# Kernel optimization log

Hardware: AMD Instinct MI355X
Metric: run time of the kernel (lower is better)

## Reference

```python
import jax, jax.numpy as jnp
import numpy as np

B, C, D, H, W = 4, 256, 16, 16, 16
REDUCTION = 8
CR = C // REDUCTION  # q/k channel dim = 32


def setup_inputs() -> dict:
    key = jax.random.key(0)
    k1, k2, k3, k4, k5, k6 = jax.random.split(key, 6)
    x = jax.random.normal(k1, (B, C, D, H, W), dtype=jnp.float32)
    # 1x1x1 conv weights are just [out_ch, in_ch] matrices
    Wq = jax.random.normal(k2, (CR, C), dtype=jnp.float32) * (1.0 / np.sqrt(C))
    Wk = jax.random.normal(k3, (CR, C), dtype=jnp.float32) * (1.0 / np.sqrt(C))
    Wv = jax.random.normal(k4, (C, C), dtype=jnp.float32) * (1.0 / np.sqrt(C))
    Wo = jax.random.normal(k5, (C, C), dtype=jnp.float32) * (1.0 / np.sqrt(C))
    gamma = jnp.zeros((1,), dtype=jnp.float32) + 0.5  # nonzero so output depends on attention
    return {"x": x, "Wq": Wq, "Wk": Wk, "Wv": Wv, "Wo": Wo, "gamma": gamma}


def reference(x, Wq, Wk, Wv, Wo, gamma):
    b, c, d, h, w = x.shape
    n = d * h * w
    scale = Wq.shape[0] ** -0.5  # (channels // reduction) ** -0.5
    xf = x.reshape(b, c, n)                      # [B, C, N]
    q = jnp.einsum('oc,bcn->bon', Wq, xf)        # [B, CR, N]
    k = jnp.einsum('oc,bcn->bon', Wk, xf)        # [B, CR, N]
    v = jnp.einsum('oc,bcn->bon', Wv, xf)        # [B, C, N]
    attn = jax.nn.softmax(jnp.einsum('bcn,bcm->bnm', q, k) * scale, axis=-1)  # [B, N, N]
    out = jnp.einsum('bcm,bnm->bcn', v, attn)    # v @ attn^T -> [B, C, N]
    out = jnp.einsum('oc,bcn->bon', Wo, out)     # output 1x1x1 conv
    out = out.reshape(b, c, d, h, w)
    return gamma[0] * out + x
```

## Files before the change

### kernel.cpp

```cpp
#include <hip/hip_runtime.h>
#include <hip/hip_bf16.h>

#define BATCH 4
#define CH 256
#define CRD 32
#define NN 4096

typedef __bf16 bf16x8 __attribute__((ext_vector_type(8)));
typedef float floatx4 __attribute__((ext_vector_type(4)));
typedef float floatx16 __attribute__((ext_vector_type(16)));
typedef unsigned short ushort4v __attribute__((ext_vector_type(4)));
typedef unsigned short ushort8v __attribute__((ext_vector_type(8)));
typedef unsigned int uint2v __attribute__((ext_vector_type(2)));
typedef unsigned int uint4v __attribute__((ext_vector_type(4)));

static __device__ __forceinline__ unsigned short f2bf(float f) {
    __bf16 h = (__bf16)f;
    return __builtin_bit_cast(unsigned short, h);
}
static __device__ __forceinline__ float bf2f(unsigned short h) {
    return __uint_as_float((unsigned int)h << 16);
}


__global__ __launch_bounds__(256) void wconv_kernel(
    const float* __restrict__ Wq, const float* __restrict__ Wk,
    const float* __restrict__ Wv, const float* __restrict__ Wo,
    unsigned short* __restrict__ What, unsigned short* __restrict__ WobF)
{
    const int o = blockIdx.x;
    const int t = threadIdx.x;
    float scale = 1.0f;
    const float* src;
    if (o < 32)      { src = Wq + o * 256;
                       scale = 0.17677669529663687f * 1.4426950408889634f; }
    else if (o < 64) { src = Wk + (o - 32) * 256; }
    else             { src = Wv + (o - 64) * 256; }
    const int mb = o >> 5;
    const size_t idx = ((size_t)(mb * 16 + (t >> 4)) * 64
                        + (o & 31) + 32 * ((t >> 3) & 1)) * 8 + (t & 7);
    What[idx] = f2bf(src[t] * scale);
    if (o < 256) {
        const size_t i2 = ((size_t)((o >> 5) * 16 + (t >> 4)) * 64
                           + (o & 31) + 32 * ((t >> 3) & 1)) * 8 + (t & 7);
        WobF[i2] = f2bf(Wo[o * 256 + t]);
    }
}

static __device__ __forceinline__ uint4v hmerge(
    const ushort4v& xp, const ushort4v& yp, int h)
{
    uint2v xd = __builtin_bit_cast(uint2v, xp);
    uint2v yd = __builtin_bit_cast(uint2v, yp);
    unsigned int px0 = (unsigned int)__shfl_xor((int)xd[0], 32);
    unsigned int px1 = (unsigned int)__shfl_xor((int)xd[1], 32);
    unsigned int py0 = (unsigned int)__shfl_xor((int)yd[0], 32);
    unsigned int py1 = (unsigned int)__shfl_xor((int)yd[1], 32);
    uint4v st;
    st[0] = h ? py0 : xd[0];
    st[1] = h ? py1 : xd[1];
    st[2] = h ? yd[0] : px0;
    st[3] = h ? yd[1] : px1;
    return st;
}

__global__ __launch_bounds__(256, 2) void qkv_kernel(
    const float* __restrict__ x, const unsigned short* __restrict__ What,
    unsigned short* __restrict__ qh, unsigned short* __restrict__ kh,
    unsigned short* __restrict__ vh)
{
    __shared__ __align__(16) unsigned short xf[16 * 512];

    const int t = threadIdx.x;
    const int w = t >> 6;
    const int l = t & 63;
    const int l31 = l & 31;
    const int h = l >> 5;
    const int nt = blockIdx.x, b = blockIdx.y;
    const int n0 = nt * 32;

    {
        const float* xb = x + (size_t)(b * CH) * NN + n0;
        const int n = t & 31;
        const int cq = t >> 5;
        #pragma unroll
        for (int p = 0; p < 8; ++p) {
            int c = p * 32 + cq * 4;
            float v0 = xb[(size_t)(c + 0) * NN + n];
            float v1 = xb[(size_t)(c + 1) * NN + n];
            float v2 = xb[(size_t)(c + 2) * NN + n];
            float v3 = xb[(size_t)(c + 3) * NN + n];
            ushort4v u4;
            u4[0] = f2bf(v0); u4[1] = f2bf(v1); u4[2] = f2bf(v2); u4[3] = f2bf(v3);
            int addr = ((2 * p + (cq >> 2)) * 64 + n + 32 * ((cq >> 1) & 1)) * 8
                       + 4 * (cq & 1);
            *(ushort4v*)&xf[addr] = u4;
        }
    }
    __syncthreads();

    const int mb0 = w, mb1 = w + 4, mb2 = w + 8;
    floatx16 acc0, acc1, acc2;
    #pragma unroll
    for (int i = 0; i < 16; ++i) { acc0[i] = 0.f; acc1[i] = 0.f; acc2[i] = 0.f; }

    for (int kblk = 0; kblk < 16; ++kblk) {
        bf16x8 bf = *(const bf16x8*)&xf[kblk * 512 + l * 8];
        bf16x8 a0 = *(const bf16x8*)(What + ((size_t)(mb0 * 16 + kblk) * 64 + l) * 8);
        bf16x8 a1 = *(const bf16x8*)(What + ((size_t)(mb1 * 16 + kblk) * 64 + l) * 8);
        acc0 = __builtin_amdgcn_mfma_f32_32x32x16_bf16(a0, bf, acc0, 0, 0, 0);
        acc1 = __builtin_amdgcn_mfma_f32_32x32x16_bf16(a1, bf, acc1, 0, 0, 0);
        if (w < 2) {
            bf16x8 a2 = *(const bf16x8*)(What + ((size_t)(mb2 * 16 + kblk) * 64 + l) * 8);
            acc2 = __builtin_amdgcn_mfma_f32_32x32x16_bf16(a2, bf, acc2, 0, 0, 0);
        }
    }

    auto store_qk = [&](unsigned short* dst, const floatx16& a) {
        size_t base = (size_t)(b * 128 + nt) * 1024;
        #pragma unroll
        for (int sb = 0; sb < 2; ++sb) {
            ushort4v xp, yp;
            #pragma unroll
            for (int i = 0; i < 4; ++i) {
                xp[i] = f2bf(a[8 * sb + i]);
                yp[i] = f2bf(a[8 * sb + 4 + i]);
            }
            uint4v st = hmerge(xp, yp, h);
            *(uint4v*)(dst + base + (size_t)sb * 512 + (size_t)l * 8) = st;
        }
    };

    if (w == 0)      store_qk(qh, acc0);
    else if (w == 1) store_qk(kh, acc0);

    __syncthreads();

    auto store_v_lds = [&](int cblk, const floatx16& a) {
        const int chunk = cblk * 2 + (l31 >> 4);
        const int hib = (l31 >> 3) & 1;
        #pragma unroll
        for (int r = 0; r < 16; ++r) {
            int rowo = (r & 3) + 8 * (r >> 2) + 4 * h;
            int unit = chunk * 64 + hib * 32 + rowo;
            int pu = unit ^ ((unit >> 5) & 7);
            xf[pu * 8 + (l31 & 7)] = f2bf(a[r]);
        }
    };

    if (w >= 2) store_v_lds(w - 2, acc0);
    store_v_lds(w + 2, acc1);
    if (w < 2) store_v_lds(w + 6, acc2);

    __syncthreads();

    #pragma unroll
    for (int p = 0; p < 4; ++p) {
        int Lu = p * 256 + t;
        int pu = Lu ^ ((Lu >> 5) & 7);
        uint4v d = *(const uint4v*)&xf[pu * 8];
        int chunk = Lu >> 6;
        int cblk = chunk >> 1, sub = chunk & 1;
        size_t dst = (((size_t)b * 8 + cblk) * 256 + nt * 2 + sub) * 512
                     + (size_t)(Lu & 63) * 8;
        *(uint4v*)(vh + dst) = d;
    }
}

#define SM_M0 12.0f

__global__ __launch_bounds__(512, 4) void attn_kernel(
    const unsigned short* __restrict__ qh, const unsigned short* __restrict__ kh,
    const unsigned short* __restrict__ vh, unsigned short* __restrict__ Opart,
    float* __restrict__ ml)
{
    __shared__ unsigned short p_lds[2 * 16 * 64 * 8];
    __shared__ float psum_s[8][32];

    const int t = threadIdx.x;
    const int w = t >> 6;
    const int l = t & 63;
    const int l31 = l & 31;
    const int h = l >> 5;
    const int wk = w & 3;
    const int hq = w >> 2;

    const int lin = blockIdx.x + ((int)blockIdx.y << 6) + ((int)blockIdx.z << 7);
    const int combo = lin & 7;
    const int gp = lin >> 3;
    const int ks = combo & 1;
    const int b  = combo >> 1;
    const int g0 = 2 * gp, g1 = 2 * gp + 1;

    const unsigned short* qB = qh + (size_t)(b * 128 + (hq ? g1 : g0)) * 1024;
    const unsigned short* kB = kh + (size_t)b * 128 * 1024;
    const unsigned short* vB = vh + (size_t)b * 8 * 256 * 512;

    bf16x8 qf0 = *(const bf16x8*)(qB + l * 8);
    bf16x8 qf1 = *(const bf16x8*)(qB + 512 + l * 8);

    bf16x8 kf0 = *(const bf16x8*)(kB + (size_t)(ks * 64 + wk) * 1024 + l * 8);
    bf16x8 kf1 = *(const bf16x8*)(kB + (size_t)(ks * 64 + wk) * 1024 + 512 + l * 8);

    float l_loc = 0.f;
    floatx16 acc_a, acc_b;
    #pragma unroll
    for (int i = 0; i < 16; ++i) { acc_a[i] = 0.f; acc_b[i] = 0.f; }

    for (int it = 0; it < 16; ++it) {
        const int pbase = (it & 1) << 13;

        floatx16 sacc;
        #pragma unroll
        for (int i = 0; i < 16; ++i) sacc[i] = 0.f;
        __builtin_amdgcn_s_setprio(1);
        sacc = __builtin_amdgcn_mfma_f32_32x32x16_bf16(kf0, qf0, sacc, 0, 0, 0);
        sacc = __builtin_amdgcn_mfma_f32_32x32x16_bf16(kf1, qf1, sacc, 0, 0, 0);
        __builtin_amdgcn_s_setprio(0);

        float pv[16];
        #pragma unroll
        for (int r = 0; r < 16; ++r) pv[r] = __builtin_exp2f(sacc[r] - SM_M0);
        float s0 = (pv[0] + pv[1]) + (pv[2] + pv[3]);
        float s1 = (pv[4] + pv[5]) + (pv[6] + pv[7]);
        float s2 = (pv[8] + pv[9]) + (pv[10] + pv[11]);
        float s3 = (pv[12] + pv[13]) + (pv[14] + pv[15]);
        l_loc += (s0 + s1) + (s2 + s3);
        #pragma unroll
        for (int rg = 0; rg < 4; ++rg) {
            ushort4v pk;
            #pragma unroll
            for (int i = 0; i < 4; ++i) pk[i] = f2bf(pv[rg * 4 + i]);
            int idx = pbase
                    + ((hq * 8 + 2 * wk + (rg >> 1)) * 64
                       + l31 + 32 * (rg & 1)) * 8 + 4 * h;
            *(ushort4v*)&p_lds[idx] = pk;
        }
        if (it < 15) {
            const unsigned short* kn = kB + (size_t)(ks * 64 + (it + 1) * 4 + wk) * 1024;
            kf0 = *(const bf16x8*)(kn + l * 8);
            kf1 = *(const bf16x8*)(kn + 512 + l * 8);
        }
        const unsigned short* v0b = vB + ((size_t)w * 256 + (ks * 16 + it) * 8) * 512;
        bf16x8 va0 = *(const bf16x8*)(v0b + 0 * 512 + l * 8);
        bf16x8 va1 = *(const bf16x8*)(v0b + 1 * 512 + l * 8);
        bf16x8 va2 = *(const bf16x8*)(v0b + 2 * 512 + l * 8);
        bf16x8 va3 = *(const bf16x8*)(v0b + 3 * 512 + l * 8);
        bf16x8 va4 = *(const bf16x8*)(v0b + 4 * 512 + l * 8);
        bf16x8 va5 = *(const bf16x8*)(v0b + 5 * 512 + l * 8);
        bf16x8 va6 = *(const bf16x8*)(v0b + 6 * 512 + l * 8);
        bf16x8 va7 = *(const bf16x8*)(v0b + 7 * 512 + l * 8);

        __syncthreads();

        bf16x8 pa = *(const bf16x8*)&p_lds[pbase + l * 8];
        bf16x8 pb = *(const bf16x8*)&p_lds[pbase + 4096 + l * 8];
        #pragma unroll
        for (int s = 0; s < 8; ++s) {
            bf16x8 vcur = (s == 0) ? va0 : (s == 1) ? va1 : (s == 2) ? va2
                        : (s == 3) ? va3 : (s == 4) ? va4 : (s == 5) ? va5
                        : (s == 6) ? va6 : va7;
            bf16x8 pa_n, pb_n;
            if (s < 7) {
                pa_n = *(const bf16x8*)&p_lds[pbase + ((s + 1) * 64 + l) * 8];
                pb_n = *(const bf16x8*)&p_lds[pbase + 4096 + ((s + 1) * 64 + l) * 8];
            }
            __builtin_amdgcn_s_setprio(1);
            acc_a = __builtin_amdgcn_mfma_f32_32x32x16_bf16(vcur, pa, acc_a, 0, 0, 0);
            acc_b = __builtin_amdgcn_mfma_f32_32x32x16_bf16(vcur, pb, acc_b, 0, 0, 0);
            __builtin_amdgcn_s_setprio(0);
            pa = pa_n; pb = pb_n;
        }
    }

    float lt = l_loc + __shfl_xor(l_loc, 32);
    if (h == 0) psum_s[w][l31] = lt;
    __syncthreads();

    if (w == 0 && h == 0) {
        float l_run = (psum_s[0][l31] + psum_s[1][l31])
                    + (psum_s[2][l31] + psum_s[3][l31]);
        ml[((size_t)(b * 128 + g0) * 2 + ks) * 32 + l31] = l_run;
    }
    if (w == 4 && h == 0) {
        float l_run = (psum_s[4][l31] + psum_s[5][l31])
                    + (psum_s[6][l31] + psum_s[7][l31]);
        ml[((size_t)(b * 128 + g1) * 2 + ks) * 32 + l31] = l_run;
    }

    unsigned short* opa = Opart + ((size_t)((b * 128 + g0) * 2 + ks)) * 8192;
    unsigned short* opb = Opart + ((size_t)((b * 128 + g1) * 2 + ks)) * 8192;
    #pragma unroll
    for (int ct = 0; ct < 2; ++ct) {
        const floatx16& a = ct ? acc_b : acc_a;
        unsigned short* op = ct ? opb : opa;
        #pragma unroll
        for (int sb = 0; sb < 2; ++sb) {
            ushort4v xp, yp;
            #pragma unroll
            for (int i = 0; i < 4; ++i) {
                xp[i] = f2bf(a[8 * sb + i]);
                yp[i] = f2bf(a[8 * sb + 4 + i]);
            }
            uint4v st = hmerge(xp, yp, h);
            int sP = 2 * w + sb;
            *(uint4v*)(op + ((size_t)sP * 64 + l) * 8) = st;
        }
    }
}

__global__ __launch_bounds__(256, 2) void out_kernel(
    const unsigned short* __restrict__ Opart, const float* __restrict__ ml,
    const unsigned short* __restrict__ WobF, const float* __restrict__ x,
    const float* __restrict__ gamma, float* __restrict__ out)
{
    const int t = threadIdx.x;
    const int w = t >> 6;
    const int l = t & 63;
    const int l31 = l & 31;
    const int h = l >> 5;
    const int qt = blockIdx.x, b = blockIdx.y;

    const size_t slot2 = (size_t)(b * 128 + qt) * 2;
    float l0 = ml[(slot2 + 0) * 32 + l31];
    float l1 = ml[(slot2 + 1) * 32 + l31];
    float rL = 1.0f / (l0 + l1);

    const unsigned short* o0 = Opart + (slot2 + 0) * 8192;
    const unsigned short* o1 = Opart + (slot2 + 1) * 8192;

    floatx16 a0[2], a1[2];
    #pragma unroll
    for (int m = 0; m < 2; ++m)
        #pragma unroll
        for (int i = 0; i < 16; ++i) { a0[m][i] = 0.f; a1[m][i] = 0.f; }

    #pragma unroll 2
    for (int s = 0; s < 16; ++s) {
        bf16x8 f0 = *(const bf16x8*)(o0 + (s * 64 + l) * 8);
        bf16x8 f1 = *(const bf16x8*)(o1 + (s * 64 + l) * 8);
        #pragma unroll
        for (int m = 0; m < 2; ++m) {
            int mt = 2 * w + m;
            bf16x8 af = *(const bf16x8*)(WobF + ((size_t)(mt * 16 + s) * 64 + l) * 8);
            a0[m] = __builtin_amdgcn_mfma_f32_32x32x16_bf16(af, f0, a0[m], 0, 0, 0);
            a1[m] = __builtin_amdgcn_mfma_f32_32x32x16_bf16(af, f1, a1[m], 0, 0, 0);
        }
    }

    const float gm = gamma[0];
    #pragma unroll
    for (int m = 0; m < 2; ++m)
        #pragma unroll
        for (int r = 0; r < 16; ++r) {
            float v = (a0[m][r] + a1[m][r]) * rL;
            int o = (2 * w + m) * 32 + (r & 3) + 8 * (r >> 2) + 4 * h;
            int n = qt * 32 + l31;
            size_t oi = ((size_t)(b * 256 + o)) * NN + n;
            out[oi] = gm * v + x[oi];
        }
}

extern "C" void kernel_launch(void* const* d_in, const int* in_sizes, int n_in,
                              void* d_out, int out_size, void* d_ws, size_t ws_size,
                              hipStream_t stream)
{
    const float* x     = (const float*)d_in[0];
    const float* Wq    = (const float*)d_in[1];
    const float* Wk    = (const float*)d_in[2];
    const float* Wv    = (const float*)d_in[3];
    const float* Wo    = (const float*)d_in[4];
    const float* gamma = (const float*)d_in[5];
    float* out = (float*)d_out;

    char* wsb = (char*)d_ws;
    unsigned short* qh    = (unsigned short*)(wsb);
    unsigned short* kh    = (unsigned short*)(wsb + (1u << 20));
    unsigned short* vh    = (unsigned short*)(wsb + (2u << 20));
    unsigned short* What  = (unsigned short*)(wsb + (10u << 20));
    unsigned short* WobF  = (unsigned short*)(wsb + (10u << 20) + (256u << 10));
    unsigned short* Opart = (unsigned short*)(wsb + (11u << 20));
    float*          ml    = (float*)         (wsb + (45u << 20));

    wconv_kernel<<<320, 256, 0, stream>>>(Wq, Wk, Wv, Wo, What, WobF);

    dim3 g1(128, BATCH);
    qkv_kernel<<<g1, 256, 0, stream>>>(x, What, qh, kh, vh);

    dim3 g2(64, 2, BATCH);
    attn_kernel<<<g2, 512, 0, stream>>>(qh, kh, vh, Opart, ml);

    dim3 g3(128, BATCH);
    out_kernel<<<g3, 256, 0, stream>>>(Opart, ml, WobF, x, gamma, out);
}
```

Baseline: 150.9 us.

## Spread QKV and output projection work across more waves and blocks

The QKV kernel now launches 640 threads (10 waves), so each wave computes a single 32-row tile instead of two or three. The x load and V writeback are split across 512 threads. The output kernel's grid is doubled along a new y dimension so each wave handles one output tile instead of two. The intent is more parallelism and occupancy for these small kernels, in exchange for redundant Opart and x loads across blocks and larger block sizes.

```diff
diff --git a/kernel.cpp b/kernel.cpp
--- a/kernel.cpp
+++ b/kernel.cpp
@@ -64,7 +64,7 @@
     return st;
 }
 
-__global__ __launch_bounds__(256, 2) void qkv_kernel(
+__global__ __launch_bounds__(640, 4) void qkv_kernel(
     const float* __restrict__ x, const unsigned short* __restrict__ What,
     unsigned short* __restrict__ qh, unsigned short* __restrict__ kh,
     unsigned short* __restrict__ vh)
@@ -79,41 +79,34 @@
     const int nt = blockIdx.x, b = blockIdx.y;
     const int n0 = nt * 32;
 
-    {
+    if (t < 512) {
         const float* xb = x + (size_t)(b * CH) * NN + n0;
         const int n = t & 31;
         const int cq = t >> 5;
         #pragma unroll
-        for (int p = 0; p < 8; ++p) {
-            int c = p * 32 + cq * 4;
+        for (int p = 0; p < 4; ++p) {
+            int c = p * 64 + cq * 4;
             float v0 = xb[(size_t)(c + 0) * NN + n];
             float v1 = xb[(size_t)(c + 1) * NN + n];
             float v2 = xb[(size_t)(c + 2) * NN + n];
             float v3 = xb[(size_t)(c + 3) * NN + n];
             ushort4v u4;
             u4[0] = f2bf(v0); u4[1] = f2bf(v1); u4[2] = f2bf(v2); u4[3] = f2bf(v3);
-            int addr = ((2 * p + (cq >> 2)) * 64 + n + 32 * ((cq >> 1) & 1)) * 8
+            int addr = ((4 * p + (cq >> 2)) * 64 + n + 32 * ((cq >> 1) & 1)) * 8
                        + 4 * (cq & 1);
             *(ushort4v*)&xf[addr] = u4;
         }
     }
     __syncthreads();
 
-    const int mb0 = w, mb1 = w + 4, mb2 = w + 8;
-    floatx16 acc0, acc1, acc2;
-    #pragma unroll
-    for (int i = 0; i < 16; ++i) { acc0[i] = 0.f; acc1[i] = 0.f; acc2[i] = 0.f; }
+    floatx16 acc;
+    #pragma unroll
+    for (int i = 0; i < 16; ++i) acc[i] = 0.f;
 
     for (int kblk = 0; kblk < 16; ++kblk) {
         bf16x8 bf = *(const bf16x8*)&xf[kblk * 512 + l * 8];
-        bf16x8 a0 = *(const bf16x8*)(What + ((size_t)(mb0 * 16 + kblk) * 64 + l) * 8);
-        bf16x8 a1 = *(const bf16x8*)(What + ((size_t)(mb1 * 16 + kblk) * 64 + l) * 8);
-        acc0 = __builtin_amdgcn_mfma_f32_32x32x16_bf16(a0, bf, acc0, 0, 0, 0);
-        acc1 = __builtin_amdgcn_mfma_f32_32x32x16_bf16(a1, bf, acc1, 0, 0, 0);
-        if (w < 2) {
-            bf16x8 a2 = *(const bf16x8*)(What + ((size_t)(mb2 * 16 + kblk) * 64 + l) * 8);
-            acc2 = __builtin_amdgcn_mfma_f32_32x32x16_bf16(a2, bf, acc2, 0, 0, 0);
-        }
+        bf16x8 af = *(const bf16x8*)(What + ((size_t)(w * 16 + kblk) * 64 + l) * 8);
+        acc = __builtin_amdgcn_mfma_f32_32x32x16_bf16(af, bf, acc, 0, 0, 0);
     }
 
     auto store_qk = [&](unsigned short* dst, const floatx16& a) {
@@ -131,12 +124,13 @@
         }
     };
 
-    if (w == 0)      store_qk(qh, acc0);
-    else if (w == 1) store_qk(kh, acc0);
+    if (w == 0)      store_qk(qh, acc);
+    else if (w == 1) store_qk(kh, acc);
 
     __syncthreads();
 
-    auto store_v_lds = [&](int cblk, const floatx16& a) {
+    if (w >= 2) {
+        const int cblk = w - 2;
         const int chunk = cblk * 2 + (l31 >> 4);
         const int hib = (l31 >> 3) & 1;
         #pragma unroll
@@ -144,26 +138,24 @@
             int rowo = (r & 3) + 8 * (r >> 2) + 4 * h;
             int unit = chunk * 64 + hib * 32 + rowo;
             int pu = unit ^ ((unit >> 5) & 7);
-            xf[pu * 8 + (l31 & 7)] = f2bf(a[r]);
-        }
-    };
-
-    if (w >= 2) store_v_lds(w - 2, acc0);
-    store_v_lds(w + 2, acc1);
-    if (w < 2) store_v_lds(w + 6, acc2);
+            xf[pu * 8 + (l31 & 7)] = f2bf(acc[r]);
+        }
+    }
 
     __syncthreads();
 
-    #pragma unroll
-    for (int p = 0; p < 4; ++p) {
-        int Lu = p * 256 + t;
-        int pu = Lu ^ ((Lu >> 5) & 7);
-        uint4v d = *(const uint4v*)&xf[pu * 8];
-        int chunk = Lu >> 6;
-        int cblk = chunk >> 1, sub = chunk & 1;
-        size_t dst = (((size_t)b * 8 + cblk) * 256 + nt * 2 + sub) * 512
-                     + (size_t)(Lu & 63) * 8;
-        *(uint4v*)(vh + dst) = d;
+    if (t < 512) {
+        #pragma unroll
+        for (int p = 0; p < 2; ++p) {
+            int Lu = p * 512 + t;
+            int pu = Lu ^ ((Lu >> 5) & 7);
+            uint4v d = *(const uint4v*)&xf[pu * 8];
+            int chunk = Lu >> 6;
+            int cblk = chunk >> 1, sub = chunk & 1;
+            size_t dst = (((size_t)b * 8 + cblk) * 256 + nt * 2 + sub) * 512
+                         + (size_t)(Lu & 63) * 8;
+            *(uint4v*)(vh + dst) = d;
+        }
     }
 }
 
@@ -309,7 +301,7 @@
     }
 }
 
-__global__ __launch_bounds__(256, 2) void out_kernel(
+__global__ __launch_bounds__(256, 4) void out_kernel(
     const unsigned short* __restrict__ Opart, const float* __restrict__ ml,
     const unsigned short* __restrict__ WobF, const float* __restrict__ x,
     const float* __restrict__ gamma, float* __restrict__ out)
@@ -319,7 +311,8 @@
     const int l = t & 63;
     const int l31 = l & 31;
     const int h = l >> 5;
-    const int qt = blockIdx.x, b = blockIdx.y;
+    const int qt = blockIdx.x, mhalf = blockIdx.y, b = blockIdx.z;
+    const int mt = mhalf * 4 + w;
 
     const size_t slot2 = (size_t)(b * 128 + qt) * 2;
     float l0 = ml[(slot2 + 0) * 32 + l31];
@@ -329,36 +322,27 @@
     const unsigned short* o0 = Opart + (slot2 + 0) * 8192;
     const unsigned short* o1 = Opart + (slot2 + 1) * 8192;
 
-    floatx16 a0[2], a1[2];
-    #pragma unroll
-    for (int m = 0; m < 2; ++m)
-        #pragma unroll
-        for (int i = 0; i < 16; ++i) { a0[m][i] = 0.f; a1[m][i] = 0.f; }
-
-    #pragma unroll 2
+    floatx16 a0, a1;
+    #pragma unroll
+    for (int i = 0; i < 16; ++i) { a0[i] = 0.f; a1[i] = 0.f; }
+
     for (int s = 0; s < 16; ++s) {
         bf16x8 f0 = *(const bf16x8*)(o0 + (s * 64 + l) * 8);
         bf16x8 f1 = *(const bf16x8*)(o1 + (s * 64 + l) * 8);
-        #pragma unroll
-        for (int m = 0; m < 2; ++m) {
-            int mt = 2 * w + m;
-            bf16x8 af = *(const bf16x8*)(WobF + ((size_t)(mt * 16 + s) * 64 + l) * 8);
-            a0[m] = __builtin_amdgcn_mfma_f32_32x32x16_bf16(af, f0, a0[m], 0, 0, 0);
-            a1[m] = __builtin_amdgcn_mfma_f32_32x32x16_bf16(af, f1, a1[m], 0, 0, 0);
-        }
+        bf16x8 af = *(const bf16x8*)(WobF + ((size_t)(mt * 16 + s) * 64 + l) * 8);
+        a0 = __builtin_amdgcn_mfma_f32_32x32x16_bf16(af, f0, a0, 0, 0, 0);
+        a1 = __builtin_amdgcn_mfma_f32_32x32x16_bf16(af, f1, a1, 0, 0, 0);
     }
 
     const float gm = gamma[0];
     #pragma unroll
-    for (int m = 0; m < 2; ++m)
-        #pragma unroll
-        for (int r = 0; r < 16; ++r) {
-            float v = (a0[m][r] + a1[m][r]) * rL;
-            int o = (2 * w + m) * 32 + (r & 3) + 8 * (r >> 2) + 4 * h;
-            int n = qt * 32 + l31;
-            size_t oi = ((size_t)(b * 256 + o)) * NN + n;
-            out[oi] = gm * v + x[oi];
-        }
+    for (int r = 0; r < 16; ++r) {
+        float v = (a0[r] + a1[r]) * rL;
+        int o = mt * 32 + (r & 3) + 8 * (r >> 2) + 4 * h;
+        int n = qt * 32 + l31;
+        size_t oi = ((size_t)(b * 256 + o)) * NN + n;
+        out[oi] = gm * v + x[oi];
+    }
 }
 
 extern "C" void kernel_launch(void* const* d_in, const int* in_sizes, int n_in,
@@ -385,11 +369,11 @@
     wconv_kernel<<<320, 256, 0, stream>>>(Wq, Wk, Wv, Wo, What, WobF);
 
     dim3 g1(128, BATCH);
-    qkv_kernel<<<g1, 256, 0, stream>>>(x, What, qh, kh, vh);
+    qkv_kernel<<<g1, 640, 0, stream>>>(x, What, qh, kh, vh);
 
     dim3 g2(64, 2, BATCH);
     attn_kernel<<<g2, 512, 0, stream>>>(qh, kh, vh, Opart, ml);
 
-    dim3 g3(128, BATCH);
+    dim3 g3(128, 2, BATCH);
     out_kernel<<<g3, 256, 0, stream>>>(Opart, ml, WobF, x, gamma, out);
 }
```

New measurement: 136.9 us, median of 4. 1.1x faster.
